# Optimization experiments

Hardware: AMD Instinct MI355X
Metric: run time of the kernel (lower is better)

Reference implementation:

```python
import jax, jax.numpy as jnp
import numpy as np
from jax import lax

B, L, D = 16, 512, 512          # batch, sequence length, embed dim
CB = 4096                        # codebook size
SCALES = (1, 2, 4, 8, 16, 32, 64, 128, 256, 512)
K_PHI = 4                        # number of partially-shared Phi convs
RESI = 0.5                       # abs(quant_resi)
KS = 3                           # Phi conv kernel size
# PhiPartiallyShared tick selection (K==4 branch): linspace(1/12, 11/12, 4)
_ticks = np.linspace(1.0 / 3 / K_PHI, 1.0 - 1.0 / 3 / K_PHI, K_PHI)
PHI_IDX = tuple(int(np.argmin(np.abs(_ticks - si / (len(SCALES) - 1)))) for si in range(len(SCALES)))


def setup_inputs() -> dict:
    key = jax.random.key(0)
    k1, k2, k3 = jax.random.split(key, 3)
    x = jax.random.normal(k1, (B, L, D), dtype=jnp.float32)
    embed = jax.random.normal(k2, (CB, D), dtype=jnp.float32)          # EuclideanCodebook.embed
    phi_w = jax.random.normal(k3, (K_PHI, D, D, KS), dtype=jnp.float32) * (1.0 / np.sqrt(D * KS))
    phi_b = jnp.zeros((K_PHI, D), dtype=jnp.float32)
    return {"x": x, "embed": embed, "phi_w": phi_w, "phi_b": phi_b}


def _phi(h_bcl, w, b):
    # Phi.forward: h*(1-r) + conv1d(h)*r ; h is [B, C, L]
    conv = lax.conv_general_dilated(h_bcl, w, window_strides=(1,),
                                    padding=[(KS // 2, KS // 2)],
                                    dimension_numbers=("NCH", "OIH", "NCH"))
    conv = conv + b[None, :, None]
    return h_bcl * (1.0 - RESI) + conv * RESI


def reference(x, embed, phi_w, phi_b):
    e_sq = jnp.sum(embed * embed, axis=-1)  # [CB]
    f_hat = jnp.zeros_like(x)
    residual = x
    for si, s in enumerate(SCALES):
        # F.interpolate(mode='area') down to s == exact block mean (L % s == 0)
        z = residual.reshape(B, s, L // s, D).mean(axis=2)  # [B, s, D]
        # Euclidean quantize: argmin ||z - e||^2  (same as argmax of -dist in torch)
        dist = jnp.sum(z * z, axis=-1, keepdims=True) - 2.0 * jnp.einsum("bsd,cd->bsc", z, embed) + e_sq
        idx = jnp.argmin(dist, axis=-1)       # [B, s]
        q = embed[idx]                        # dequantize, [B, s, D]
        qc = jnp.transpose(q, (0, 2, 1))      # [B, D, s]
        if s != L:
            # F.interpolate(mode='linear', align_corners=False) -> half-pixel linear
            qc = jax.image.resize(qc, (B, D, L), method="linear")
        qc = _phi(qc, phi_w[PHI_IDX[si]], phi_b[PHI_IDX[si]])
        q_up = jnp.transpose(qc, (0, 2, 1))   # [B, L, D]
        f_hat = f_hat + q_up
        residual = residual - q_up
    return f_hat
```

## Files before the change

kernel.cpp:

```cpp
#include <hip/hip_runtime.h>


#define ND 512
#define NCB 4096
#define DELTA 0.5f

typedef _Float16 half8v __attribute__((ext_vector_type(8)));
typedef float floatx4 __attribute__((ext_vector_type(4)));

struct HL { _Float16 h, l; };

__device__ __forceinline__ HL split2(float v) {
    HL r;
    r.h = (_Float16)v;
    r.l = (_Float16)((v - (float)r.h) * 4096.0f);
    return r;
}

__device__ __forceinline__ unsigned long long pack_dist(float d, int n) {
    unsigned u = __float_as_uint(d);
    u = (u & 0x80000000u) ? ~u : (u | 0x80000000u);
    return ((unsigned long long)u << 32) | (unsigned)n;
}

__device__ __forceinline__ float unpack_dist(unsigned long long p) {
    unsigned u = (unsigned)(p >> 32);
    u = (u & 0x80000000u) ? (u & 0x7fffffffu) : ~u;
    return __uint_as_float(u);
}

__device__ __forceinline__ void gl2lds16(const _Float16* g, _Float16* l) {
    __builtin_amdgcn_global_load_lds(
        (const __attribute__((address_space(1))) unsigned int*)g,
        (__attribute__((address_space(3))) unsigned int*)l, 16, 0, 0);
}

__global__ __launch_bounds__(256) void k_prep_embed(const float* __restrict__ embed,
        _Float16* __restrict__ eh, _Float16* __restrict__ el, float* __restrict__ esq) {
    int c = blockIdx.x * 4 + (threadIdx.x >> 6);
    int lane = threadIdx.x & 63;
    const float* row = embed + (size_t)c * ND + lane * 8;
    float4 v0 = *(const float4*)row;
    float4 v1 = *(const float4*)(row + 4);
    float vs[8] = {v0.x, v0.y, v0.z, v0.w, v1.x, v1.y, v1.z, v1.w};
    half8v h8, l8;
    double acc = 0.0;
#pragma unroll
    for (int i = 0; i < 8; ++i) {
        HL r = split2(vs[i]);
        h8[i] = r.h; l8[i] = r.l;
        acc += (double)vs[i] * (double)vs[i];
    }
    *(half8v*)(eh + (size_t)c * ND + lane * 8) = h8;
    *(half8v*)(el + (size_t)c * ND + lane * 8) = l8;
#pragma unroll
    for (int off = 32; off > 0; off >>= 1) acc += __shfl_down(acc, off, 64);
    if (lane == 0) esq[c] = (float)acc;
}

__global__ __launch_bounds__(256) void k_split_w(const float* __restrict__ pw,
        _Float16* __restrict__ wh, _Float16* __restrict__ wl) {
    int gid = blockIdx.x * 256 + threadIdx.x;
    int din = gid & 511;
    int nn = (gid >> 9) % 1536;
    int kp = gid / (512 * 1536);
    int tap = nn >> 9;
    int dout = nn & 511;
    float v = pw[(((size_t)(kp * 512 + dout) * 512) + din) * 3 + tap];
    HL r = split2(v);
    wh[gid] = r.h;
    wl[gid] = r.l;
}

__global__ __launch_bounds__(256) void k_zmean(const float* __restrict__ src,
        _Float16* __restrict__ zh, _Float16* __restrict__ zl, int s, int lg) {
    int gid = blockIdx.x * 256 + threadIdx.x;
    int d = gid & 511;
    int j = (gid >> 9) & (s - 1);
    int b = gid >> (9 + lg);
    int r = 512 >> lg;
    const float* p = src + ((size_t)((b << 9) + (j << (9 - lg))) << 9) + d;
    double acc = 0.0;
#pragma unroll 4
    for (int m = 0; m < r; ++m) acc += (double)p[(size_t)m * ND];
    float v = (float)(acc * (1.0 / (double)r));
    HL hl = split2(v);
    zh[gid] = hl.h;
    zl[gid] = hl.l;
}

__global__ __launch_bounds__(256) void k_zmean_s(const float* __restrict__ src,
        _Float16* __restrict__ zh, _Float16* __restrict__ zl, int s, int lg) {
    int bj = blockIdx.x >> 3;
    int dblk = blockIdx.x & 7;
    int b = bj >> lg;
    int j = bj & (s - 1);
    int wave = threadIdx.x >> 6, lane = threadIdx.x & 63;
    int rg = lane >> 4;
    int dl = lane & 15;
    int d = dblk * 64 + wave * 16 + dl;
    int r = 512 >> lg;
    const float* p = src + ((size_t)((b << 9) + (j << (9 - lg))) << 9) + d;
    double acc = 0.0;
    for (int k = rg; k < r; k += 4) acc += (double)p[(size_t)k * ND];
    acc += __shfl_down(acc, 32, 64);
    acc += __shfl_down(acc, 16, 64);
    if (rg == 0) {
        float v = (float)(acc * (1.0 / (double)r));
        HL hl = split2(v);
        size_t gi = ((size_t)bj << 9) + d;
        zh[gi] = hl.h;
        zl[gi] = hl.l;
    }
}

__global__ __launch_bounds__(256, 4) void k_dist1(const _Float16* __restrict__ zh,
        const _Float16* __restrict__ eh, const float* __restrict__ esq,
        unsigned long long* __restrict__ bm2, int M) {
    __shared__ _Float16 smem[2][2][4096] __attribute__((aligned(16)));
    unsigned long long (*packs2)[2][2] =
        reinterpret_cast<unsigned long long(*)[2][2]>(&smem[0][0][0]);
    int tid = threadIdx.x;
    int lane = tid & 63, wave = tid >> 6;
    int wm = wave >> 1, wn = wave & 1;
    int quad = lane >> 4, l15 = lane & 15;
    int m0 = blockIdx.x * 128, n0 = blockIdx.y * 128;

    int slot = lane & 3;
    int r0 = wave * 32 + (lane >> 2);
    int r1 = r0 + 16;
    int sc0 = (slot ^ ((r0 >> 1) & 3)) << 3;
    int sc1 = (slot ^ ((r1 >> 1) & 3)) << 3;
    int a0 = m0 + r0; if (a0 >= M) a0 = M - 1;
    int a1 = m0 + r1; if (a1 >= M) a1 = M - 1;
    const _Float16* gA0 = zh + (size_t)a0 * 512 + sc0;
    const _Float16* gA1 = zh + (size_t)a1 * 512 + sc1;
    const _Float16* gB0 = eh + (size_t)(n0 + r0) * 512 + sc0;
    const _Float16* gB1 = eh + (size_t)(n0 + r1) * 512 + sc1;
    int ld0 = wave * 1024, ld1 = ld0 + 512;

    int cslot = (quad ^ ((l15 >> 1) & 3)) << 3;
    int rbA = (wm * 64 + l15) * 32 + cslot;
    int rbB = (wn * 64 + l15) * 32 + cslot;

#define STG(buf, kb) do { \
    gl2lds16(gA0 + (kb), &smem[buf][0][ld0]); \
    gl2lds16(gA1 + (kb), &smem[buf][0][ld1]); \
    gl2lds16(gB0 + (kb), &smem[buf][1][ld0]); \
    gl2lds16(gB1 + (kb), &smem[buf][1][ld1]); \
} while (0)

    floatx4 acc[4][4];
#pragma unroll
    for (int i = 0; i < 4; ++i)
#pragma unroll
        for (int j = 0; j < 4; ++j)
#pragma unroll
            for (int r = 0; r < 4; ++r) acc[i][j][r] = 0.f;

    STG(0, 0);
    __syncthreads();
    int cur = 0;
    for (int it = 0; it < 16; ++it) {
        if (it < 15) STG(cur ^ 1, (it + 1) * 32);
        const _Float16* sA = &smem[cur][0][0];
        const _Float16* sB = &smem[cur][1][0];
        half8v af[4], bf[4];
#pragma unroll
        for (int tm = 0; tm < 4; ++tm) af[tm] = *(const half8v*)&sA[rbA + tm * 512];
#pragma unroll
        for (int tn = 0; tn < 4; ++tn) bf[tn] = *(const half8v*)&sB[rbB + tn * 512];
#pragma unroll
        for (int tm = 0; tm < 4; ++tm)
#pragma unroll
            for (int tn = 0; tn < 4; ++tn)
                acc[tm][tn] = __builtin_amdgcn_mfma_f32_16x16x32_f16(af[tm], bf[tn], acc[tm][tn], 0, 0, 0);
        __syncthreads();
        cur ^= 1;
    }
#undef STG
    float es[4];
#pragma unroll
    for (int tn = 0; tn < 4; ++tn) es[tn] = esq[n0 + wn * 64 + tn * 16 + l15];
#pragma unroll
    for (int tm = 0; tm < 4; ++tm)
#pragma unroll
        for (int reg = 0; reg < 4; ++reg) {
            unsigned long long b = ~0ull, sd = ~0ull;
#pragma unroll
            for (int tn = 0; tn < 4; ++tn) {
                float dd = fmaf(-2.f, acc[tm][tn][reg], es[tn]);
                int n = n0 + wn * 64 + tn * 16 + l15;
                unsigned long long p = pack_dist(dd, n);
                if (p < b) { sd = b; b = p; } else if (p < sd) sd = p;
            }
#pragma unroll
            for (int off = 1; off < 16; off <<= 1) {
                unsigned long long ob = __shfl_xor(b, off, 64);
                unsigned long long os = __shfl_xor(sd, off, 64);
                unsigned long long mx = b > ob ? b : ob;
                b = b < ob ? b : ob;
                unsigned long long mn2 = sd < os ? sd : os;
                sd = mx < mn2 ? mx : mn2;
            }
            if (l15 == 0) {
                packs2[wm * 64 + tm * 16 + quad * 4 + reg][wn][0] = b;
                packs2[wm * 64 + tm * 16 + quad * 4 + reg][wn][1] = sd;
            }
        }
    __syncthreads();
    if (tid < 128) {
        unsigned long long b0 = packs2[tid][0][0], s0 = packs2[tid][0][1];
        unsigned long long b1 = packs2[tid][1][0], s1 = packs2[tid][1][1];
        unsigned long long b = b0 < b1 ? b0 : b1;
        unsigned long long mx = b0 > b1 ? b0 : b1;
        unsigned long long mn2 = s0 < s1 ? s0 : s1;
        unsigned long long sd = mx < mn2 ? mx : mn2;
        size_t idx = ((size_t)(m0 + tid) * 32 + blockIdx.y) * 2;
        bm2[idx] = b;
        bm2[idx + 1] = sd;
    }
}

__global__ __launch_bounds__(256) void k_refine(const _Float16* __restrict__ zh,
        const _Float16* __restrict__ zl, const float* __restrict__ embed,
        const unsigned long long* __restrict__ bm2,
        unsigned long long* __restrict__ minbuf, int M) {
    int lane = threadIdx.x & 63, wave = threadIdx.x >> 6;
    int m = blockIdx.x * 4 + wave;
    if (m >= M) return;
    float zr[8];
    const _Float16* ph = zh + (size_t)m * 512 + lane * 8;
    const _Float16* pl = zl + (size_t)m * 512 + lane * 8;
#pragma unroll
    for (int i = 0; i < 8; ++i)
        zr[i] = (float)ph[i] + (float)pl[i] * (1.0f / 4096.0f);
    unsigned long long p = bm2[(size_t)m * 64 + lane];
    unsigned long long mn = p;
#pragma unroll
    for (int off = 1; off < 64; off <<= 1) {
        unsigned long long q = __shfl_xor(mn, off, 64);
        mn = q < mn ? q : mn;
    }
    float T = unpack_dist(mn) + DELTA;
    unsigned long long mask = __ballot(unpack_dist(p) <= T);
    double bestD = 1e300;
    int bestI = 0x7fffffff;
    while (mask) {
        int bit = __ffsll((unsigned long long)mask) - 1;
        mask &= mask - 1;
        int idx = (int)(unsigned)__shfl(p, bit, 64);
        const float* e = embed + (size_t)idx * 512 + lane * 8;
        double s = 0.0;
#pragma unroll
        for (int i = 0; i < 8; ++i) {
            double df = (double)zr[i] - (double)e[i];
            s += df * df;
        }
#pragma unroll
        for (int off = 32; off > 0; off >>= 1) s += __shfl_down(s, off, 64);
        if (lane == 0) {
            if (s < bestD || (s == bestD && idx < bestI)) { bestD = s; bestI = idx; }
        }
    }
    if (lane == 0) minbuf[m] = (unsigned long long)(unsigned)bestI;
}

__global__ __launch_bounds__(256, 2) void k_phi(const _Float16* __restrict__ eh,
        const _Float16* __restrict__ el, const _Float16* __restrict__ wh,
        const _Float16* __restrict__ wl, const unsigned long long* __restrict__ minbuf,
        float* __restrict__ u, int M) {
    __shared__ _Float16 smem[2][4][4096] __attribute__((aligned(16)));
    int* idxs = reinterpret_cast<int*>(&smem[0][0][0]);
    int tid = threadIdx.x;
    int lane = tid & 63, wave = tid >> 6;
    int wm = wave >> 1, wn = wave & 1;
    int quad = lane >> 4, l15 = lane & 15;
    int m0 = blockIdx.x * 128, n0 = blockIdx.y * 128;
    if (tid < 128) {
        int m = m0 + tid; if (m >= M) m = M - 1;
        idxs[tid] = (int)(unsigned)minbuf[m];
    }
    __syncthreads();

    int slot = lane & 3;
    int r0 = wave * 32 + (lane >> 2);
    int r1 = r0 + 16;
    int sc0 = (slot ^ ((r0 >> 1) & 3)) << 3;
    int sc1 = (slot ^ ((r1 >> 1) & 3)) << 3;
    int code0 = idxs[r0];
    int code1 = idxs[r1];
    __syncthreads();
    const _Float16* gA0h = eh + (size_t)code0 * 512 + sc0;
    const _Float16* gA1h = eh + (size_t)code1 * 512 + sc1;
    const _Float16* gA0l = el + (size_t)code0 * 512 + sc0;
    const _Float16* gA1l = el + (size_t)code1 * 512 + sc1;
    const _Float16* gB0h = wh + (size_t)(n0 + r0) * 512 + sc0;
    const _Float16* gB1h = wh + (size_t)(n0 + r1) * 512 + sc1;
    const _Float16* gB0l = wl + (size_t)(n0 + r0) * 512 + sc0;
    const _Float16* gB1l = wl + (size_t)(n0 + r1) * 512 + sc1;
    int ld0 = wave * 1024;
    int ld1 = ld0 + 512;

    int cslot = (quad ^ ((l15 >> 1) & 3)) << 3;
    int rbA = (wm * 64 + l15) * 32 + cslot;
    int rbB = (wn * 64 + l15) * 32 + cslot;

#define STAGE_P(buf, kb) do { \
    gl2lds16(gA0h + (kb), &smem[buf][0][ld0]); \
    gl2lds16(gA1h + (kb), &smem[buf][0][ld1]); \
    gl2lds16(gA0l + (kb), &smem[buf][1][ld0]); \
    gl2lds16(gA1l + (kb), &smem[buf][1][ld1]); \
    gl2lds16(gB0h + (kb), &smem[buf][2][ld0]); \
    gl2lds16(gB1h + (kb), &smem[buf][2][ld1]); \
    gl2lds16(gB0l + (kb), &smem[buf][3][ld0]); \
    gl2lds16(gB1l + (kb), &smem[buf][3][ld1]); \
} while (0)

    floatx4 acch[4][4], accx[4][4];
#pragma unroll
    for (int i = 0; i < 4; ++i)
#pragma unroll
        for (int j = 0; j < 4; ++j)
#pragma unroll
            for (int r = 0; r < 4; ++r) { acch[i][j][r] = 0.f; accx[i][j][r] = 0.f; }

    STAGE_P(0, 0);
    __syncthreads();
    int cur = 0;
    for (int it = 0; it < 16; ++it) {
        if (it < 15) STAGE_P(cur ^ 1, (it + 1) * 32);
        const _Float16* sAh = &smem[cur][0][0];
        const _Float16* sAl = &smem[cur][1][0];
        const _Float16* sBh = &smem[cur][2][0];
        const _Float16* sBl = &smem[cur][3][0];
        half8v afh[4], afl[4], bfh[4], bfl[4];
#pragma unroll
        for (int tm = 0; tm < 4; ++tm) {
            afh[tm] = *(const half8v*)&sAh[rbA + tm * 512];
            afl[tm] = *(const half8v*)&sAl[rbA + tm * 512];
        }
#pragma unroll
        for (int tn = 0; tn < 4; ++tn) {
            bfh[tn] = *(const half8v*)&sBh[rbB + tn * 512];
            bfl[tn] = *(const half8v*)&sBl[rbB + tn * 512];
        }
#pragma unroll
        for (int tm = 0; tm < 4; ++tm)
#pragma unroll
            for (int tn = 0; tn < 4; ++tn) {
                acch[tm][tn] = __builtin_amdgcn_mfma_f32_16x16x32_f16(afh[tm], bfh[tn], acch[tm][tn], 0, 0, 0);
                accx[tm][tn] = __builtin_amdgcn_mfma_f32_16x16x32_f16(afh[tm], bfl[tn], accx[tm][tn], 0, 0, 0);
                accx[tm][tn] = __builtin_amdgcn_mfma_f32_16x16x32_f16(afl[tm], bfh[tn], accx[tm][tn], 0, 0, 0);
            }
        __syncthreads();
        cur ^= 1;
    }
#undef STAGE_P
#pragma unroll
    for (int tm = 0; tm < 4; ++tm)
#pragma unroll
        for (int reg = 0; reg < 4; ++reg) {
            int m = m0 + wm * 64 + tm * 16 + quad * 4 + reg;
            if (m < M) {
#pragma unroll
                for (int tn = 0; tn < 4; ++tn) {
                    int n = n0 + wn * 64 + tn * 16 + l15;
                    u[(size_t)m * 1536 + n] = acch[tm][tn][reg] + accx[tm][tn][reg] * (1.0f / 4096.0f);
                }
            }
        }
}

__global__ __launch_bounds__(256) void k_combine(const float* __restrict__ u,
        const float* __restrict__ embed, const unsigned long long* __restrict__ minbuf,
        const float* __restrict__ bias, const float* __restrict__ rsrc,
        float* __restrict__ resid, int s, float scale) {
    int tid = threadIdx.x;
    int m = blockIdx.x * 2 + (tid >> 7);
    int d4 = (tid & 127) << 2;
    int b = m >> 9, t = m & 511;
    int bs = b * s;
    float4 bi = *(const float4*)(bias + d4);
    float uu = ((float)t + 0.5f) * scale - 0.5f;
    float fl = floorf(uu);
    float w = uu - fl;
    int i0 = (int)fl, i1 = i0 + 1;
    i0 = min(max(i0, 0), s - 1);
    i1 = min(max(i1, 0), s - 1);
    int c0 = (int)(unsigned)minbuf[bs + i0];
    int c1 = (int)(unsigned)minbuf[bs + i1];
    float4 e0 = *(const float4*)(embed + (size_t)c0 * 512 + d4);
    float4 e1 = *(const float4*)(embed + (size_t)c1 * 512 + d4);
    float om = 1.0f - w;
    float4 h4;
    h4.x = om * e0.x + w * e1.x; h4.y = om * e0.y + w * e1.y;
    h4.z = om * e0.z + w * e1.z; h4.w = om * e0.w + w * e1.w;
    float4 conv = make_float4(0.f, 0.f, 0.f, 0.f);
#pragma unroll
    for (int tap = 0; tap < 3; ++tap) {
        int tt = t + tap - 1;
        if (tt >= 0 && tt < 512) {
            float uu2 = ((float)tt + 0.5f) * scale - 0.5f;
            float fl2 = floorf(uu2);
            float w2 = uu2 - fl2;
            int j0 = (int)fl2, j1 = j0 + 1;
            j0 = min(max(j0, 0), s - 1);
            j1 = min(max(j1, 0), s - 1);
            float4 a4 = *(const float4*)(u + (size_t)(bs + j0) * 1536 + tap * 512 + d4);
            float4 b4 = *(const float4*)(u + (size_t)(bs + j1) * 1536 + tap * 512 + d4);
            float ow = 1.0f - w2;
            conv.x += ow * a4.x + w2 * b4.x;
            conv.y += ow * a4.y + w2 * b4.y;
            conv.z += ow * a4.z + w2 * b4.z;
            conv.w += ow * a4.w + w2 * b4.w;
        }
    }
    size_t off = (size_t)m * 512 + d4;
    float4 rv = *(const float4*)(rsrc + off);
    rv.x -= 0.5f * h4.x + 0.5f * (conv.x + bi.x);
    rv.y -= 0.5f * h4.y + 0.5f * (conv.y + bi.y);
    rv.z -= 0.5f * h4.z + 0.5f * (conv.z + bi.z);
    rv.w -= 0.5f * h4.w + 0.5f * (conv.w + bi.w);
    *(float4*)(resid + off) = rv;
}

__global__ __launch_bounds__(256) void k_prep_q(const float* __restrict__ embed,
        const unsigned long long* __restrict__ minbuf, _Float16* __restrict__ qh,
        _Float16* __restrict__ ql, int s, float scale, _Float16* __restrict__ zbuf) {
    int gid = blockIdx.x * 256 + threadIdx.x;
    if (gid < 1024) zbuf[gid] = (_Float16)0.f;
    int d8 = (gid & 63) << 3;
    int m = gid >> 6;
    int b = m >> 9, t = m & 511;
    int bs = b * s;
    float uu = ((float)t + 0.5f) * scale - 0.5f;
    float fl = floorf(uu);
    float w = uu - fl;
    int i0 = (int)fl, i1 = i0 + 1;
    i0 = min(max(i0, 0), s - 1);
    i1 = min(max(i1, 0), s - 1);
    int c0 = (int)(unsigned)minbuf[bs + i0];
    int c1 = (int)(unsigned)minbuf[bs + i1];
    const float* p0 = embed + (size_t)c0 * 512 + d8;
    const float* p1 = embed + (size_t)c1 * 512 + d8;
    float ow = 1.0f - w;
    half8v hh8, ll8;
#pragma unroll
    for (int q = 0; q < 8; ++q) {
        float v = ow * p0[q] + w * p1[q];
        HL hl = split2(v);
        hh8[q] = hl.h; ll8[q] = hl.l;
    }
    *(half8v*)(qh + (size_t)m * 512 + d8) = hh8;
    *(half8v*)(ql + (size_t)m * 512 + d8) = ll8;
}

__global__ __launch_bounds__(256, 2) void k_conv(const _Float16* __restrict__ qh,
        const _Float16* __restrict__ ql, const float* __restrict__ embed,
        const _Float16* __restrict__ wh, const _Float16* __restrict__ wl,
        const float* __restrict__ bias, const unsigned long long* __restrict__ minbuf,
        float* __restrict__ resid, int s, float scale,
        const float* __restrict__ x, float* __restrict__ out, int last,
        const _Float16* __restrict__ zbuf) {
    __shared__ _Float16 smem[2][12288] __attribute__((aligned(16)));
    int tid = threadIdx.x;
    int lane = tid & 63, wave = tid >> 6;
    int wm = wave >> 1, wn = wave & 1;
    int quad = lane >> 4, l15 = lane & 15;
    int m0 = blockIdx.x * 128, n0 = blockIdx.y * 64;
    int b = m0 >> 9, t0 = m0 & 511;
    int rw = wave * 16 + (lane >> 2);
    int slot = lane & 3;
    int scA0 = (slot ^ ((rw >> 1) & 3)) << 3;
    int scA1 = (slot ^ (((rw + 64) >> 1) & 3)) << 3;
    int ldw = wave * 512;

#define MKP(T) \
    int tp0_##T = t0 + rw + (T) - 1; \
    int tp1_##T = tp0_##T + 64; \
    const _Float16* aH0_##T = ((unsigned)tp0_##T < 512u) ? qh + (((size_t)((b << 9) + tp0_##T)) << 9) + scA0 : zbuf + scA0; \
    const _Float16* aL0_##T = ((unsigned)tp0_##T < 512u) ? ql + (((size_t)((b << 9) + tp0_##T)) << 9) + scA0 : zbuf + scA0; \
    const _Float16* aH1_##T = ((unsigned)tp1_##T < 512u) ? qh + (((size_t)((b << 9) + tp1_##T)) << 9) + scA1 : zbuf + scA1; \
    const _Float16* aL1_##T = ((unsigned)tp1_##T < 512u) ? ql + (((size_t)((b << 9) + tp1_##T)) << 9) + scA1 : zbuf + scA1; \
    const _Float16* bH_##T = wh + (((size_t)(((T) << 9) + n0 + rw)) << 9) + scA0; \
    const _Float16* bL_##T = wl + (((size_t)(((T) << 9) + n0 + rw)) << 9) + scA0;
    MKP(0)
    MKP(1)
    MKP(2)
#undef MKP

#define STG_T(buf, T, dkh) do { \
    gl2lds16(aH0_##T + (dkh), &smem[buf][ldw]); \
    gl2lds16(aH1_##T + (dkh), &smem[buf][2048 + ldw]); \
    gl2lds16(aL0_##T + (dkh), &smem[buf][4096 + ldw]); \
    gl2lds16(aL1_##T + (dkh), &smem[buf][6144 + ldw]); \
    gl2lds16(bH_##T + (dkh), &smem[buf][8192 + ldw]); \
    gl2lds16(bL_##T + (dkh), &smem[buf][10240 + ldw]); \
} while (0)

    floatx4 acch[4][2], accx[4][2];
#pragma unroll
    for (int i = 0; i < 4; ++i)
#pragma unroll
        for (int j = 0; j < 2; ++j)
#pragma unroll
            for (int r = 0; r < 4; ++r) { acch[i][j][r] = 0.f; accx[i][j][r] = 0.f; }

    STG_T(0, 0, 0);
    __syncthreads();
    int cur = 0;
    for (int it = 0; it < 48; ++it) {
        int nit = it + 1;
        int ndk = (nit & 15) << 5;
        if (nit < 16) STG_T(cur ^ 1, 0, ndk);
        else if (nit < 32) STG_T(cur ^ 1, 1, ndk);
        else if (nit < 48) STG_T(cur ^ 1, 2, ndk);
        const _Float16* sb = &smem[cur][0];
        half8v afh[4], afl[4], bfh[2], bfl[2];
#pragma unroll
        for (int tm = 0; tm < 4; ++tm) {
            int rA = wm * 64 + tm * 16 + l15;
            int cs = (quad ^ ((rA >> 1) & 3)) << 3;
            afh[tm] = *(const half8v*)&sb[rA * 32 + cs];
            afl[tm] = *(const half8v*)&sb[4096 + rA * 32 + cs];
        }
#pragma unroll
        for (int tn = 0; tn < 2; ++tn) {
            int rB = wn * 32 + tn * 16 + l15;
            int cs = (quad ^ ((rB >> 1) & 3)) << 3;
            bfh[tn] = *(const half8v*)&sb[8192 + rB * 32 + cs];
            bfl[tn] = *(const half8v*)&sb[10240 + rB * 32 + cs];
        }
#pragma unroll
        for (int tm = 0; tm < 4; ++tm)
#pragma unroll
            for (int tn = 0; tn < 2; ++tn) {
                acch[tm][tn] = __builtin_amdgcn_mfma_f32_16x16x32_f16(afh[tm], bfh[tn], acch[tm][tn], 0, 0, 0);
                accx[tm][tn] = __builtin_amdgcn_mfma_f32_16x16x32_f16(afh[tm], bfl[tn], accx[tm][tn], 0, 0, 0);
                accx[tm][tn] = __builtin_amdgcn_mfma_f32_16x16x32_f16(afl[tm], bfh[tn], accx[tm][tn], 0, 0, 0);
            }
        __syncthreads();
        cur ^= 1;
    }
#undef STG_T
#pragma unroll
    for (int tm = 0; tm < 4; ++tm)
#pragma unroll
        for (int reg = 0; reg < 4; ++reg) {
            int rrow = wm * 64 + tm * 16 + quad * 4 + reg;
            int m = m0 + rrow;
            int t = t0 + rrow;
            float uu = ((float)t + 0.5f) * scale - 0.5f;
            float fl = floorf(uu);
            float w = uu - fl;
            int i0 = (int)fl, i1 = i0 + 1;
            i0 = min(max(i0, 0), s - 1);
            i1 = min(max(i1, 0), s - 1);
            int bs = b * s;
            int c0 = (int)(unsigned)minbuf[bs + i0];
            int c1 = (int)(unsigned)minbuf[bs + i1];
            float ow = 1.0f - w;
#pragma unroll
            for (int tn = 0; tn < 2; ++tn) {
                int n = n0 + wn * 32 + tn * 16 + l15;
                float h = ow * embed[(size_t)c0 * 512 + n] + w * embed[(size_t)c1 * 512 + n];
                float val = acch[tm][tn][reg] + accx[tm][tn][reg] * (1.0f / 4096.0f);
                size_t off = (size_t)m * 512 + n;
                float r2 = resid[off] - (0.5f * h + 0.5f * (val + bias[n]));
                if (last) out[off] = x[off] - r2;
                else resid[off] = r2;
            }
        }
}

extern "C" void kernel_launch(void* const* d_in, const int* in_sizes, int n_in,
                              void* d_out, int out_size, void* d_ws, size_t ws_size,
                              hipStream_t stream) {
    const float* x     = (const float*)d_in[0];
    const float* embed = (const float*)d_in[1];
    const float* pw    = (const float*)d_in[2];
    const float* pb    = (const float*)d_in[3];
    float* out = (float*)d_out;

    float* resid = (float*)d_ws;
    float* Ubase = resid + 4194304;
    _Float16* zh = (_Float16*)Ubase;
    _Float16* zl = zh + 4194304;
    float* u = Ubase;
    _Float16* ehi = (_Float16*)(Ubase + 4194304);
    _Float16* elo = ehi + 2097152;
    _Float16* whi = elo + 2097152;
    _Float16* wlo = whi + 3145728;
    float* esq = (float*)(wlo + 3145728);
    unsigned long long* minbuf = (unsigned long long*)(esq + 4096);
    unsigned long long* bm2 = (unsigned long long*)(minbuf + 8192);
    _Float16* zbuf = (_Float16*)(bm2 + 524288);

    k_prep_embed<<<1024, 256, 0, stream>>>(embed, ehi, elo, esq);
    k_split_w<<<12288, 256, 0, stream>>>(pw, whi, wlo);

    const int SCv[10] = {1, 2, 4, 8, 16, 32, 64, 128, 256, 512};
    const int PIv[10] = {0, 0, 1, 1, 1, 2, 2, 3, 3, 3};
    for (int si = 0; si < 10; ++si) {
        int s = SCv[si];
        int M = 16 * s;
        int kp = PIv[si];
        int lg = __builtin_ctz((unsigned)s);
        float scale = (float)s / 512.0f;
        const float* src = (si == 0) ? x : resid;
        if (s <= 8)
            k_zmean_s<<<16 * s * 8, 256, 0, stream>>>(src, zh, zl, s, lg);
        else
            k_zmean<<<(M * 512) / 256, 256, 0, stream>>>(src, zh, zl, s, lg);
        k_dist1<<<dim3((M + 127) / 128, 32), 256, 0, stream>>>(zh, ehi, esq, bm2, M);
        k_refine<<<(M + 3) / 4, 256, 0, stream>>>(zh, zl, embed, bm2, minbuf, M);
        if (s <= 128) {
            k_phi<<<dim3((M + 127) / 128, 12), 256, 0, stream>>>(ehi, elo,
                    whi + (size_t)kp * 1536 * 512, wlo + (size_t)kp * 1536 * 512, minbuf, u, M);
            k_combine<<<4096, 256, 0, stream>>>(u, embed, minbuf, pb + kp * 512, src, resid, s, scale);
        } else {
            k_prep_q<<<2048, 256, 0, stream>>>(embed, minbuf, zh, zl, s, scale, zbuf);
            k_conv<<<dim3(64, 8), 256, 0, stream>>>(zh, zl, embed,
                    whi + (size_t)kp * 1536 * 512, wlo + (size_t)kp * 1536 * 512,
                    pb + kp * 512, minbuf, resid, s, scale, x, out, si == 9 ? 1 : 0, zbuf);
        }
    }
}
```

Before: 820.1 us.

## Precompute codebook-times-Phi table once for last three scales, replace per-scale conv GEMM

The last three scales (128, 256, 512) all use Phi index 3. The new k_pmat kernel computes, once, the product of every codebook entry with the three conv taps (4096x1536) and stores it as a hi/lo fp16 split. k_combineP then builds each scale's conv output by gathering and interpolating rows of that table, replacing the per-scale prep_q plus full conv GEMM. This trades two large B*L GEMMs for one codebook-sized GEMM plus gather-heavy combines. It reuses d_out and the weight buffers as scratch, which needs a separate final kernel for the output and overwrites the split weights of Phi slots 0 and 1 after they are no longer needed.

Result: faster. 740.0 us (-9.8%).

```diff
diff --git a/kernel.cpp b/kernel.cpp
--- a/kernel.cpp
+++ b/kernel.cpp
@@ -6,6 +6,7 @@
 #define DELTA 0.5f
 
 typedef _Float16 half8v __attribute__((ext_vector_type(8)));
+typedef _Float16 half4v __attribute__((ext_vector_type(4)));
 typedef float floatx4 __attribute__((ext_vector_type(4)));
 
 struct HL { _Float16 h, l; };
@@ -33,6 +34,19 @@
     __builtin_amdgcn_global_load_lds(
         (const __attribute__((address_space(1))) unsigned int*)g,
         (__attribute__((address_space(3))) unsigned int*)l, 16, 0, 0);
+}
+
+__device__ __forceinline__ _Float16* plrow(_Float16* p0, _Float16* p1,
+                                           _Float16* p2, int c) {
+    return c < 1536 ? p0 + (size_t)c * 1536
+         : c < 3072 ? p1 + (size_t)(c - 1536) * 1536
+                    : p2 + (size_t)(c - 3072) * 1536;
+}
+__device__ __forceinline__ const _Float16* plrowc(const _Float16* p0,
+        const _Float16* p1, const _Float16* p2, int c) {
+    return c < 1536 ? p0 + (size_t)c * 1536
+         : c < 3072 ? p1 + (size_t)(c - 1536) * 1536
+                    : p2 + (size_t)(c - 3072) * 1536;
 }
 
 __global__ __launch_bounds__(256) void k_prep_embed(const float* __restrict__ embed,
@@ -368,6 +382,108 @@
                     int n = n0 + wn * 64 + tn * 16 + l15;
                     u[(size_t)m * 1536 + n] = acch[tm][tn][reg] + accx[tm][tn][reg] * (1.0f / 4096.0f);
                 }
+            }
+        }
+}
+
+__global__ __launch_bounds__(256, 2) void k_pmat(const _Float16* __restrict__ eh,
+        const _Float16* __restrict__ el, const _Float16* __restrict__ wh,
+        const _Float16* __restrict__ wl, _Float16* __restrict__ Ph,
+        _Float16* __restrict__ Pl0, _Float16* __restrict__ Pl1,
+        _Float16* __restrict__ Pl2) {
+    __shared__ _Float16 smem[2][4][4096] __attribute__((aligned(16)));
+    int tid = threadIdx.x;
+    int lane = tid & 63, wave = tid >> 6;
+    int wm = wave >> 1, wn = wave & 1;
+    int quad = lane >> 4, l15 = lane & 15;
+    int m0 = blockIdx.x * 128, n0 = blockIdx.y * 128;
+
+    int slot = lane & 3;
+    int r0 = wave * 32 + (lane >> 2);
+    int r1 = r0 + 16;
+    int sc0 = (slot ^ ((r0 >> 1) & 3)) << 3;
+    int sc1 = (slot ^ ((r1 >> 1) & 3)) << 3;
+    int code0 = m0 + r0;
+    int code1 = m0 + r1;
+    const _Float16* gA0h = eh + (size_t)code0 * 512 + sc0;
+    const _Float16* gA1h = eh + (size_t)code1 * 512 + sc1;
+    const _Float16* gA0l = el + (size_t)code0 * 512 + sc0;
+    const _Float16* gA1l = el + (size_t)code1 * 512 + sc1;
+    const _Float16* gB0h = wh + (size_t)(n0 + r0) * 512 + sc0;
+    const _Float16* gB1h = wh + (size_t)(n0 + r1) * 512 + sc1;
+    const _Float16* gB0l = wl + (size_t)(n0 + r0) * 512 + sc0;
+    const _Float16* gB1l = wl + (size_t)(n0 + r1) * 512 + sc1;
+    int ld0 = wave * 1024;
+    int ld1 = ld0 + 512;
+
+    int cslot = (quad ^ ((l15 >> 1) & 3)) << 3;
+    int rbA = (wm * 64 + l15) * 32 + cslot;
+    int rbB = (wn * 64 + l15) * 32 + cslot;
+
+#define STAGE_M(buf, kb) do { \
+    gl2lds16(gA0h + (kb), &smem[buf][0][ld0]); \
+    gl2lds16(gA1h + (kb), &smem[buf][0][ld1]); \
+    gl2lds16(gA0l + (kb), &smem[buf][1][ld0]); \
+    gl2lds16(gA1l + (kb), &smem[buf][1][ld1]); \
+    gl2lds16(gB0h + (kb), &smem[buf][2][ld0]); \
+    gl2lds16(gB1h + (kb), &smem[buf][2][ld1]); \
+    gl2lds16(gB0l + (kb), &smem[buf][3][ld0]); \
+    gl2lds16(gB1l + (kb), &smem[buf][3][ld1]); \
+} while (0)
+
+    floatx4 acch[4][4], accx[4][4];
+#pragma unroll
+    for (int i = 0; i < 4; ++i)
+#pragma unroll
+        for (int j = 0; j < 4; ++j)
+#pragma unroll
+            for (int r = 0; r < 4; ++r) { acch[i][j][r] = 0.f; accx[i][j][r] = 0.f; }
+
+    STAGE_M(0, 0);
+    __syncthreads();
+    int cur = 0;
+    for (int it = 0; it < 16; ++it) {
+        if (it < 15) STAGE_M(cur ^ 1, (it + 1) * 32);
+        const _Float16* sAh = &smem[cur][0][0];
+        const _Float16* sAl = &smem[cur][1][0];
+        const _Float16* sBh = &smem[cur][2][0];
+        const _Float16* sBl = &smem[cur][3][0];
+        half8v afh[4], afl[4], bfh[4], bfl[4];
+#pragma unroll
+        for (int tm = 0; tm < 4; ++tm) {
+            afh[tm] = *(const half8v*)&sAh[rbA + tm * 512];
+            afl[tm] = *(const half8v*)&sAl[rbA + tm * 512];
+        }
+#pragma unroll
+        for (int tn = 0; tn < 4; ++tn) {
+            bfh[tn] = *(const half8v*)&sBh[rbB + tn * 512];
+            bfl[tn] = *(const half8v*)&sBl[rbB + tn * 512];
+        }
+#pragma unroll
+        for (int tm = 0; tm < 4; ++tm)
+#pragma unroll
+            for (int tn = 0; tn < 4; ++tn) {
+                acch[tm][tn] = __builtin_amdgcn_mfma_f32_16x16x32_f16(afh[tm], bfh[tn], acch[tm][tn], 0, 0, 0);
+                accx[tm][tn] = __builtin_amdgcn_mfma_f32_16x16x32_f16(afh[tm], bfl[tn], accx[tm][tn], 0, 0, 0);
+                accx[tm][tn] = __builtin_amdgcn_mfma_f32_16x16x32_f16(afl[tm], bfh[tn], accx[tm][tn], 0, 0, 0);
+            }
+        __syncthreads();
+        cur ^= 1;
+    }
+#undef STAGE_M
+#pragma unroll
+    for (int tm = 0; tm < 4; ++tm)
+#pragma unroll
+        for (int reg = 0; reg < 4; ++reg) {
+            int m = m0 + wm * 64 + tm * 16 + quad * 4 + reg;
+            _Float16* plr = plrow(Pl0, Pl1, Pl2, m);
+#pragma unroll
+            for (int tn = 0; tn < 4; ++tn) {
+                int n = n0 + wn * 64 + tn * 16 + l15;
+                float val = acch[tm][tn][reg] + accx[tm][tn][reg] * (1.0f / 4096.0f);
+                HL r = split2(val);
+                Ph[(size_t)m * 1536 + n] = r.h;
+                plr[n] = r.l;
             }
         }
 }
@@ -425,15 +541,18 @@
     *(float4*)(resid + off) = rv;
 }
 
-__global__ __launch_bounds__(256) void k_prep_q(const float* __restrict__ embed,
-        const unsigned long long* __restrict__ minbuf, _Float16* __restrict__ qh,
-        _Float16* __restrict__ ql, int s, float scale, _Float16* __restrict__ zbuf) {
-    int gid = blockIdx.x * 256 + threadIdx.x;
-    if (gid < 1024) zbuf[gid] = (_Float16)0.f;
-    int d8 = (gid & 63) << 3;
-    int m = gid >> 6;
+__global__ __launch_bounds__(256) void k_combineP(const _Float16* __restrict__ Ph,
+        const _Float16* __restrict__ Pl0, const _Float16* __restrict__ Pl1,
+        const _Float16* __restrict__ Pl2,
+        const float* __restrict__ embed, const unsigned long long* __restrict__ minbuf,
+        const float* __restrict__ bias, const float* __restrict__ rsrc,
+        float* __restrict__ resid, int s, float scale) {
+    int tid = threadIdx.x;
+    int m = blockIdx.x * 2 + (tid >> 7);
+    int d4 = (tid & 127) << 2;
     int b = m >> 9, t = m & 511;
     int bs = b * s;
+    float4 bi = *(const float4*)(bias + d4);
     float uu = ((float)t + 0.5f) * scale - 0.5f;
     float fl = floorf(uu);
     float w = uu - fl;
@@ -442,136 +561,58 @@
     i1 = min(max(i1, 0), s - 1);
     int c0 = (int)(unsigned)minbuf[bs + i0];
     int c1 = (int)(unsigned)minbuf[bs + i1];
-    const float* p0 = embed + (size_t)c0 * 512 + d8;
-    const float* p1 = embed + (size_t)c1 * 512 + d8;
-    float ow = 1.0f - w;
-    half8v hh8, ll8;
-#pragma unroll
-    for (int q = 0; q < 8; ++q) {
-        float v = ow * p0[q] + w * p1[q];
-        HL hl = split2(v);
-        hh8[q] = hl.h; ll8[q] = hl.l;
-    }
-    *(half8v*)(qh + (size_t)m * 512 + d8) = hh8;
-    *(half8v*)(ql + (size_t)m * 512 + d8) = ll8;
-}
-
-__global__ __launch_bounds__(256, 2) void k_conv(const _Float16* __restrict__ qh,
-        const _Float16* __restrict__ ql, const float* __restrict__ embed,
-        const _Float16* __restrict__ wh, const _Float16* __restrict__ wl,
-        const float* __restrict__ bias, const unsigned long long* __restrict__ minbuf,
-        float* __restrict__ resid, int s, float scale,
-        const float* __restrict__ x, float* __restrict__ out, int last,
-        const _Float16* __restrict__ zbuf) {
-    __shared__ _Float16 smem[2][12288] __attribute__((aligned(16)));
-    int tid = threadIdx.x;
-    int lane = tid & 63, wave = tid >> 6;
-    int wm = wave >> 1, wn = wave & 1;
-    int quad = lane >> 4, l15 = lane & 15;
-    int m0 = blockIdx.x * 128, n0 = blockIdx.y * 64;
-    int b = m0 >> 9, t0 = m0 & 511;
-    int rw = wave * 16 + (lane >> 2);
-    int slot = lane & 3;
-    int scA0 = (slot ^ ((rw >> 1) & 3)) << 3;
-    int scA1 = (slot ^ (((rw + 64) >> 1) & 3)) << 3;
-    int ldw = wave * 512;
-
-#define MKP(T) \
-    int tp0_##T = t0 + rw + (T) - 1; \
-    int tp1_##T = tp0_##T + 64; \
-    const _Float16* aH0_##T = ((unsigned)tp0_##T < 512u) ? qh + (((size_t)((b << 9) + tp0_##T)) << 9) + scA0 : zbuf + scA0; \
-    const _Float16* aL0_##T = ((unsigned)tp0_##T < 512u) ? ql + (((size_t)((b << 9) + tp0_##T)) << 9) + scA0 : zbuf + scA0; \
-    const _Float16* aH1_##T = ((unsigned)tp1_##T < 512u) ? qh + (((size_t)((b << 9) + tp1_##T)) << 9) + scA1 : zbuf + scA1; \
-    const _Float16* aL1_##T = ((unsigned)tp1_##T < 512u) ? ql + (((size_t)((b << 9) + tp1_##T)) << 9) + scA1 : zbuf + scA1; \
-    const _Float16* bH_##T = wh + (((size_t)(((T) << 9) + n0 + rw)) << 9) + scA0; \
-    const _Float16* bL_##T = wl + (((size_t)(((T) << 9) + n0 + rw)) << 9) + scA0;
-    MKP(0)
-    MKP(1)
-    MKP(2)
-#undef MKP
-
-#define STG_T(buf, T, dkh) do { \
-    gl2lds16(aH0_##T + (dkh), &smem[buf][ldw]); \
-    gl2lds16(aH1_##T + (dkh), &smem[buf][2048 + ldw]); \
-    gl2lds16(aL0_##T + (dkh), &smem[buf][4096 + ldw]); \
-    gl2lds16(aL1_##T + (dkh), &smem[buf][6144 + ldw]); \
-    gl2lds16(bH_##T + (dkh), &smem[buf][8192 + ldw]); \
-    gl2lds16(bL_##T + (dkh), &smem[buf][10240 + ldw]); \
-} while (0)
-
-    floatx4 acch[4][2], accx[4][2];
-#pragma unroll
-    for (int i = 0; i < 4; ++i)
-#pragma unroll
-        for (int j = 0; j < 2; ++j)
-#pragma unroll
-            for (int r = 0; r < 4; ++r) { acch[i][j][r] = 0.f; accx[i][j][r] = 0.f; }
-
-    STG_T(0, 0, 0);
-    __syncthreads();
-    int cur = 0;
-    for (int it = 0; it < 48; ++it) {
-        int nit = it + 1;
-        int ndk = (nit & 15) << 5;
-        if (nit < 16) STG_T(cur ^ 1, 0, ndk);
-        else if (nit < 32) STG_T(cur ^ 1, 1, ndk);
-        else if (nit < 48) STG_T(cur ^ 1, 2, ndk);
-        const _Float16* sb = &smem[cur][0];
-        half8v afh[4], afl[4], bfh[2], bfl[2];
-#pragma unroll
-        for (int tm = 0; tm < 4; ++tm) {
-            int rA = wm * 64 + tm * 16 + l15;
-            int cs = (quad ^ ((rA >> 1) & 3)) << 3;
-            afh[tm] = *(const half8v*)&sb[rA * 32 + cs];
-            afl[tm] = *(const half8v*)&sb[4096 + rA * 32 + cs];
-        }
-#pragma unroll
-        for (int tn = 0; tn < 2; ++tn) {
-            int rB = wn * 32 + tn * 16 + l15;
-            int cs = (quad ^ ((rB >> 1) & 3)) << 3;
-            bfh[tn] = *(const half8v*)&sb[8192 + rB * 32 + cs];
-            bfl[tn] = *(const half8v*)&sb[10240 + rB * 32 + cs];
-        }
-#pragma unroll
-        for (int tm = 0; tm < 4; ++tm)
-#pragma unroll
-            for (int tn = 0; tn < 2; ++tn) {
-                acch[tm][tn] = __builtin_amdgcn_mfma_f32_16x16x32_f16(afh[tm], bfh[tn], acch[tm][tn], 0, 0, 0);
-                accx[tm][tn] = __builtin_amdgcn_mfma_f32_16x16x32_f16(afh[tm], bfl[tn], accx[tm][tn], 0, 0, 0);
-                accx[tm][tn] = __builtin_amdgcn_mfma_f32_16x16x32_f16(afl[tm], bfh[tn], accx[tm][tn], 0, 0, 0);
-            }
-        __syncthreads();
-        cur ^= 1;
-    }
-#undef STG_T
-#pragma unroll
-    for (int tm = 0; tm < 4; ++tm)
-#pragma unroll
-        for (int reg = 0; reg < 4; ++reg) {
-            int rrow = wm * 64 + tm * 16 + quad * 4 + reg;
-            int m = m0 + rrow;
-            int t = t0 + rrow;
-            float uu = ((float)t + 0.5f) * scale - 0.5f;
-            float fl = floorf(uu);
-            float w = uu - fl;
-            int i0 = (int)fl, i1 = i0 + 1;
-            i0 = min(max(i0, 0), s - 1);
-            i1 = min(max(i1, 0), s - 1);
-            int bs = b * s;
-            int c0 = (int)(unsigned)minbuf[bs + i0];
-            int c1 = (int)(unsigned)minbuf[bs + i1];
-            float ow = 1.0f - w;
-#pragma unroll
-            for (int tn = 0; tn < 2; ++tn) {
-                int n = n0 + wn * 32 + tn * 16 + l15;
-                float h = ow * embed[(size_t)c0 * 512 + n] + w * embed[(size_t)c1 * 512 + n];
-                float val = acch[tm][tn][reg] + accx[tm][tn][reg] * (1.0f / 4096.0f);
-                size_t off = (size_t)m * 512 + n;
-                float r2 = resid[off] - (0.5f * h + 0.5f * (val + bias[n]));
-                if (last) out[off] = x[off] - r2;
-                else resid[off] = r2;
-            }
-        }
+    float4 e0 = *(const float4*)(embed + (size_t)c0 * 512 + d4);
+    float4 e1 = *(const float4*)(embed + (size_t)c1 * 512 + d4);
+    float om = 1.0f - w;
+    float4 h4;
+    h4.x = om * e0.x + w * e1.x; h4.y = om * e0.y + w * e1.y;
+    h4.z = om * e0.z + w * e1.z; h4.w = om * e0.w + w * e1.w;
+    float4 conv = make_float4(0.f, 0.f, 0.f, 0.f);
+#pragma unroll
+    for (int tap = 0; tap < 3; ++tap) {
+        int tt = t + tap - 1;
+        if (tt >= 0 && tt < 512) {
+            float uu2 = ((float)tt + 0.5f) * scale - 0.5f;
+            float fl2 = floorf(uu2);
+            float w2 = uu2 - fl2;
+            int j0 = (int)fl2, j1 = j0 + 1;
+            j0 = min(max(j0, 0), s - 1);
+            j1 = min(max(j1, 0), s - 1);
+            int cc0 = (int)(unsigned)minbuf[bs + j0];
+            int cc1 = (int)(unsigned)minbuf[bs + j1];
+            size_t o0 = (size_t)cc0 * 1536 + tap * 512 + d4;
+            size_t oseg = tap * 512 + d4;
+            half4v ah = *(const half4v*)(Ph + o0);
+            half4v al = *(const half4v*)(plrowc(Pl0, Pl1, Pl2, cc0) + oseg);
+            half4v bh = *(const half4v*)(Ph + (size_t)cc1 * 1536 + tap * 512 + d4);
+            half4v bl = *(const half4v*)(plrowc(Pl0, Pl1, Pl2, cc1) + oseg);
+            float ow = 1.0f - w2;
+#pragma unroll
+            for (int q = 0; q < 4; ++q) {
+                float av = (float)ah[q] + (float)al[q] * (1.0f / 4096.0f);
+                float bv = (float)bh[q] + (float)bl[q] * (1.0f / 4096.0f);
+                float* cp = q == 0 ? &conv.x : q == 1 ? &conv.y : q == 2 ? &conv.z : &conv.w;
+                *cp += ow * av + w2 * bv;
+            }
+        }
+    }
+    size_t off = (size_t)m * 512 + d4;
+    float4 rv = *(const float4*)(rsrc + off);
+    rv.x -= 0.5f * h4.x + 0.5f * (conv.x + bi.x);
+    rv.y -= 0.5f * h4.y + 0.5f * (conv.y + bi.y);
+    rv.z -= 0.5f * h4.z + 0.5f * (conv.z + bi.z);
+    rv.w -= 0.5f * h4.w + 0.5f * (conv.w + bi.w);
+    *(float4*)(resid + off) = rv;
+}
+
+__global__ __launch_bounds__(256) void k_final(const float* __restrict__ x,
+        const float* __restrict__ resid, float* __restrict__ out) {
+    int gid = blockIdx.x * 256 + threadIdx.x;
+    float4 xv = ((const float4*)x)[gid];
+    float4 rv = ((const float4*)resid)[gid];
+    float4 o;
+    o.x = xv.x - rv.x; o.y = xv.y - rv.y; o.z = xv.z - rv.z; o.w = xv.w - rv.w;
+    ((float4*)out)[gid] = o;
 }
 
 extern "C" void kernel_launch(void* const* d_in, const int* in_sizes, int n_in,
@@ -595,7 +636,10 @@
     float* esq = (float*)(wlo + 3145728);
     unsigned long long* minbuf = (unsigned long long*)(esq + 4096);
     unsigned long long* bm2 = (unsigned long long*)(minbuf + 8192);
-    _Float16* zbuf = (_Float16*)(bm2 + 524288);
+    _Float16* Ph = (_Float16*)d_out;
+    _Float16* Pl0 = whi;
+    _Float16* Pl1 = wlo;
+    _Float16* Pl2 = (_Float16*)(bm2 + 524288);
 
     k_prep_embed<<<1024, 256, 0, stream>>>(embed, ehi, elo, esq);
     k_split_w<<<12288, 256, 0, stream>>>(pw, whi, wlo);
@@ -615,15 +659,18 @@
             k_zmean<<<(M * 512) / 256, 256, 0, stream>>>(src, zh, zl, s, lg);
         k_dist1<<<dim3((M + 127) / 128, 32), 256, 0, stream>>>(zh, ehi, esq, bm2, M);
         k_refine<<<(M + 3) / 4, 256, 0, stream>>>(zh, zl, embed, bm2, minbuf, M);
-        if (s <= 128) {
+        if (si <= 6) {
             k_phi<<<dim3((M + 127) / 128, 12), 256, 0, stream>>>(ehi, elo,
                     whi + (size_t)kp * 1536 * 512, wlo + (size_t)kp * 1536 * 512, minbuf, u, M);
             k_combine<<<4096, 256, 0, stream>>>(u, embed, minbuf, pb + kp * 512, src, resid, s, scale);
         } else {
-            k_prep_q<<<2048, 256, 0, stream>>>(embed, minbuf, zh, zl, s, scale, zbuf);
-            k_conv<<<dim3(64, 8), 256, 0, stream>>>(zh, zl, embed,
-                    whi + (size_t)kp * 1536 * 512, wlo + (size_t)kp * 1536 * 512,
-                    pb + kp * 512, minbuf, resid, s, scale, x, out, si == 9 ? 1 : 0, zbuf);
-        }
-    }
-}
+            if (si == 7)
+                k_pmat<<<dim3(32, 12), 256, 0, stream>>>(ehi, elo,
+                        whi + (size_t)3 * 1536 * 512, wlo + (size_t)3 * 1536 * 512,
+                        Ph, Pl0, Pl1, Pl2);
+            k_combineP<<<4096, 256, 0, stream>>>(Ph, Pl0, Pl1, Pl2, embed, minbuf,
+                    pb + 3 * 512, src, resid, s, scale);
+        }
+    }
+    k_final<<<4096, 256, 0, stream>>>(x, resid, out);
+}
```
